# Kernel tuning notes

Measured on AMD Instinct MI355X. Metric: run time of the kernel, lower is better.

## Reference

```python
import jax, jax.numpy as jnp
import numpy as np

NUM_HEADS = 16
LN_EPS = 1e-5


def setup_inputs() -> dict:
    key = jax.random.key(0)
    ks = jax.random.split(key, 7)
    B, S, D = 4, 1024, 1024
    s_in = 1.0 / np.sqrt(D)
    return {
        "x": jax.random.normal(ks[0], (B, S, D), dtype=jnp.float32),
        # PyTorch MHA packed in-projection: [3D, D] weight, [3D] bias
        "w_qkv": jax.random.uniform(ks[1], (3 * D, D), dtype=jnp.float32, minval=-s_in, maxval=s_in),
        "b_qkv": jnp.zeros((3 * D,), dtype=jnp.float32),
        "w_out": jax.random.uniform(ks[2], (D, D), dtype=jnp.float32, minval=-s_in, maxval=s_in),
        "b_out": jnp.zeros((D,), dtype=jnp.float32),
        "ln_w": jnp.ones((D,), dtype=jnp.float32),
        "ln_b": jnp.zeros((D,), dtype=jnp.float32),
    }


def _layernorm(x, w, b):
    m = jnp.mean(x, axis=-1, keepdims=True)
    v = jnp.var(x, axis=-1, keepdims=True)
    return (x - m) * jax.lax.rsqrt(v + LN_EPS) * w + b


def reference(x, w_qkv, b_qkv, w_out, b_out, ln_w, ln_b):
    B, S, D = x.shape
    H = NUM_HEADS
    hd = D // H
    # packed QKV projection (torch: F.linear(x, w_qkv, b_qkv) then chunk)
    qkv = x @ w_qkv.T + b_qkv                      # [B, S, 3D]
    q, k, v = jnp.split(qkv, 3, axis=-1)
    q = q.reshape(B, S, H, hd).transpose(0, 2, 1, 3) * (hd ** -0.5)  # [B,H,S,hd]
    k = k.reshape(B, S, H, hd).transpose(0, 2, 1, 3)
    v = v.reshape(B, S, H, hd).transpose(0, 2, 1, 3)
    scores = jnp.einsum('bhqd,bhkd->bhqk', q, k)   # [B,H,S,S]
    attn = jax.nn.softmax(scores, axis=-1)
    ctx = jnp.einsum('bhqk,bhkd->bhqd', attn, v)   # [B,H,S,hd]
    ctx = ctx.transpose(0, 2, 1, 3).reshape(B, S, D)
    attn_out = ctx @ w_out.T + b_out
    # torch returns head-averaged weights (average_attn_weights=True)
    attn_weights = attn.mean(axis=1)               # [B,S,S]
    # dropout rate 0.0 -> identity; residual + LayerNorm
    y = _layernorm(x + attn_out, ln_w, ln_b)
    return y, attn_weights
```

## Files before the change

kernel.cpp:

```cpp
#include <hip/hip_runtime.h>
#include <cstdint>

typedef __bf16 bf16;
typedef __bf16 bf16x8 __attribute__((ext_vector_type(8)));
typedef __bf16 bf16x4 __attribute__((ext_vector_type(4)));
typedef float  f32x4  __attribute__((ext_vector_type(4)));

#define MFMA_BF16(a, b, c) __builtin_amdgcn_mfma_f32_16x16x32_bf16(a, b, c, 0, 0, 0)

#define WAITCNT_VM(n) asm volatile("s_waitcnt vmcnt(" #n ")" ::: "memory")
#define CFENCE()      asm volatile("" ::: "memory")

__device__ __forceinline__ void async_load16(const void* g, void* l) {
    __builtin_amdgcn_global_load_lds(
        (__attribute__((address_space(1))) uint32_t*)(uintptr_t)g,
        (__attribute__((address_space(3))) uint32_t*)(uint32_t)(uintptr_t)l,
        16, 0, 0);
}

__global__ void cvt3_kernel(const float* __restrict__ s0, bf16* __restrict__ d0, int n0,
                            const float* __restrict__ s1, bf16* __restrict__ d1, int n1) {
    int i = blockIdx.x * blockDim.x + threadIdx.x;
    const float* s; bf16* d; int j = i;
    if (j < n0) { s = s0; d = d0; }
    else { j -= n0; if (j >= n1) return; s = s1; d = d1; }
    float4 v = ((const float4*)s)[j];
    bf16x4 o;
    o[0] = (bf16)v.x; o[1] = (bf16)v.y; o[2] = (bf16)v.z; o[3] = (bf16)v.w;
    ((bf16x4*)d)[j] = o;
}

__global__ __launch_bounds__(256) void gemm_qkv_kernel(
    const bf16* __restrict__ A, const bf16* __restrict__ W,
    const float* __restrict__ bias,
    bf16* __restrict__ Qb, bf16* __restrict__ Kb, bf16* __restrict__ Vt)
{
    const int Kd = 1024;
    __shared__ __attribute__((aligned(16))) bf16 smem[6 * 128 * 32];
    bf16* const sA0 = smem;
    bf16* const sB0 = smem + 3 * 4096;
    int tid = threadIdx.x, lane = tid & 63, wid = tid >> 6;
    int flat = blockIdx.y * 24 + blockIdx.x;
    int orig = (flat & 7) * 96 + (flat >> 3);
    int m0 = (orig / 24) * 128, n0 = (orig % 24) * 128;
    int srow = wid * 32 + (lane >> 2);
    int pchunk = lane & 3;
    int jchunk = pchunk ^ ((lane >> 3) & 3);
    const bf16* Ag = A + (size_t)(m0 + srow) * Kd + jchunk * 8;
    const bf16* Wg = W + (size_t)(n0 + srow) * Kd + jchunk * 8;
    int soff = srow * 32 + pchunk * 8;
    int wm = (wid & 1) * 64, wn = (wid >> 1) * 64;
    int lcol = lane & 15, quad = lane >> 4;
    int ckey = (lcol >> 1) & 3;
    f32x4 acc[4][4] = {};
#define STG_Q(buf, k0_) do { \
        async_load16(Ag + (k0_), sA0 + (buf) * 4096 + soff); \
        async_load16(Ag + (k0_) + 16 * Kd, sA0 + (buf) * 4096 + soff + 512); \
        async_load16(Wg + (k0_), sB0 + (buf) * 4096 + soff); \
        async_load16(Wg + (k0_) + 16 * Kd, sB0 + (buf) * 4096 + soff + 512); \
    } while (0)
    STG_Q(0, 0);
    STG_Q(1, 32);
    STG_Q(2, 64);
    int cur = 0;
    for (int it = 0; it < 32; ++it) {
        if (it < 30)      { WAITCNT_VM(8); }
        else if (it == 30){ WAITCNT_VM(4); }
        else              { WAITCNT_VM(0); }
        __builtin_amdgcn_s_barrier();
        CFENCE();
        const bf16* cA = sA0 + cur * 4096;
        const bf16* cB = sB0 + cur * 4096;
        bf16x8 af[4], bfr[4];
#pragma unroll
        for (int i = 0; i < 4; i++)
            af[i] = *(const bf16x8*)&cA[(wm + i * 16 + lcol) * 32 + (quad ^ ckey) * 8];
#pragma unroll
        for (int i = 0; i < 4; i++)
            bfr[i] = *(const bf16x8*)&cB[(wn + i * 16 + lcol) * 32 + (quad ^ ckey) * 8];
#pragma unroll
        for (int i = 0; i < 4; i++)
#pragma unroll
            for (int j = 0; j < 4; j++)
                acc[i][j] = MFMA_BF16(af[i], bfr[j], acc[i][j]);
        CFENCE();
        __builtin_amdgcn_s_barrier();
        if (it + 3 < 32) STG_Q(cur, (it + 3) * 32);
        cur = (cur == 2) ? 0 : cur + 1;
    }
#undef STG_Q
    const int LP = 136;
    bf16* sE = smem;
    int part = n0 >> 10;
    int h0 = (n0 & 1023) >> 6;
    int b = m0 >> 10, s0 = m0 & 1023;
    if (part == 2) {
#pragma unroll
        for (int j = 0; j < 4; j++) {
            float bv = bias[n0 + wn + j * 16 + lcol];
#pragma unroll
            for (int i = 0; i < 4; i++)
#pragma unroll
                for (int r = 0; r < 4; r++)
                    sE[(wn + j * 16 + lcol) * LP + (wm + i * 16 + quad * 4 + r)] = (bf16)(acc[i][j][r] + bv);
        }
        __syncthreads();
#pragma unroll
        for (int p = 0; p < 8; p++) {
            int c = p * 256 + tid;
            int nl = c >> 4, mc = (c & 15) * 8;
            int dd = nl & 63, h = h0 + (nl >> 6);
            *(bf16x8*)&Vt[(size_t)((b * 16 + h) * 64 + dd) * 1024 + s0 + mc] = *(const bf16x8*)&sE[nl * LP + mc];
        }
    } else {
        float scv = (part == 0) ? 0.125f : 1.0f;
        bf16* dst = (part == 0) ? Qb : Kb;
#pragma unroll
        for (int j = 0; j < 4; j++) {
            float bv = bias[n0 + wn + j * 16 + lcol];
#pragma unroll
            for (int i = 0; i < 4; i++)
#pragma unroll
                for (int r = 0; r < 4; r++)
                    sE[(wm + i * 16 + quad * 4 + r) * LP + (wn + j * 16 + lcol)] = (bf16)((acc[i][j][r] + bv) * scv);
        }
        __syncthreads();
#pragma unroll
        for (int p = 0; p < 8; p++) {
            int c = p * 256 + tid;
            int half = c >> 10, idx = c & 1023;
            int m = idx >> 3, nc = (idx & 7) * 8;
            *(bf16x8*)&dst[(size_t)((b * 16 + h0 + half) * 1024 + s0 + m) * 64 + nc] =
                *(const bf16x8*)&sE[m * LP + half * 64 + nc];
        }
    }
}

__global__ __launch_bounds__(256) void gemm_out_kernel(
    const bf16* __restrict__ A, const bf16* __restrict__ W,
    const float* __restrict__ bias, float* __restrict__ out)
{
    const int Kd = 1024;
    __shared__ bf16 sA[3][64 * 32];
    __shared__ bf16 sB[3][128 * 32];
    int tid = threadIdx.x, lane = tid & 63, wid = tid >> 6;
    int m0 = blockIdx.y * 64, n0 = blockIdx.x * 128;
    int ra = tid >> 2;
    int pchunk = tid & 3;
    int jchunk = pchunk ^ ((tid >> 3) & 3);
    const bf16* Ag = A + (size_t)(m0 + ra) * Kd + jchunk * 8;
    const bf16* Wg = W + (size_t)(n0 + ra) * Kd + jchunk * 8;
    int aoff = ra * 32 + pchunk * 8;
    int wm = (wid & 1) * 32, wn = (wid >> 1) * 64;
    int lcol = lane & 15, quad = lane >> 4;
    int ckey = (lcol >> 1) & 3;
    f32x4 acc[2][4] = {};
#define STG_O(buf, k0_) do { \
        async_load16(Ag + (k0_), &sA[buf][aoff]); \
        async_load16(Wg + (k0_), &sB[buf][aoff]); \
        async_load16(Wg + (k0_) + 64 * Kd, &sB[buf][aoff + 64 * 32]); \
    } while (0)
    STG_O(0, 0);
    STG_O(1, 32);
    STG_O(2, 64);
    int cur = 0;
    for (int it = 0; it < 32; ++it) {
        if (it < 30)      { WAITCNT_VM(6); }
        else if (it == 30){ WAITCNT_VM(3); }
        else              { WAITCNT_VM(0); }
        __builtin_amdgcn_s_barrier();
        CFENCE();
        const bf16* cA = sA[cur];
        const bf16* cB = sB[cur];
        bf16x8 af[2], bfr[4];
#pragma unroll
        for (int i = 0; i < 2; i++)
            af[i] = *(const bf16x8*)&cA[(wm + i * 16 + lcol) * 32 + (quad ^ ckey) * 8];
#pragma unroll
        for (int j = 0; j < 4; j++)
            bfr[j] = *(const bf16x8*)&cB[(wn + j * 16 + lcol) * 32 + (quad ^ ckey) * 8];
#pragma unroll
        for (int i = 0; i < 2; i++)
#pragma unroll
            for (int j = 0; j < 4; j++)
                acc[i][j] = MFMA_BF16(af[i], bfr[j], acc[i][j]);
        CFENCE();
        __builtin_amdgcn_s_barrier();
        if (it + 3 < 32) STG_O(cur, (it + 3) * 32);
        cur = (cur == 2) ? 0 : cur + 1;
    }
#undef STG_O
#pragma unroll
    for (int j = 0; j < 4; j++) {
        int n = n0 + wn + j * 16 + lcol;
        float bv = bias[n];
#pragma unroll
        for (int i = 0; i < 2; i++) {
            int m = m0 + wm + i * 16 + quad * 4;
#pragma unroll
            for (int r = 0; r < 4; r++) out[(size_t)(m + r) * 1024 + n] = acc[i][j][r] + bv;
        }
    }
}

__global__ __launch_bounds__(512) void flash_kernel(
    const bf16* __restrict__ Qb, const bf16* __restrict__ Kb, const bf16* __restrict__ Vt,
    bf16* __restrict__ ctx, float* __restrict__ ml)
{
    __shared__ bf16 sK[2][64 * 64];
    __shared__ bf16 sV[2][64 * 64];
    __shared__ bf16 pt[8][16 * 64];
    int tid = threadIdx.x, lane = tid & 63, wid = tid >> 6;
    int bx = blockIdx.x;
    int orig = (bx & 7) * 64 + (bx >> 3);
    int qt = orig & 7;
    int h = (orig >> 3) & 15;
    int b = orig >> 7;
    int lcol = lane & 15, quad = lane >> 4;
    size_t base = (size_t)(b * 16 + h) * 65536;

    int q0 = qt * 128 + wid * 16;
    const bf16* qp = Qb + base + (size_t)(q0 + lcol) * 64 + quad * 8;
    bf16x8 a0 = *(const bf16x8*)qp;
    bf16x8 a1 = *(const bf16x8*)(qp + 32);

    char* wpt = (char*)&pt[wid][0];
    int sr = tid >> 3;
    int pp = tid & 7;
    int jj = pp ^ (sr & 7);
    int sw = lcol & 7;

#define STAGE_KV(buf, kt_) do { \
        async_load16(Kb + base + (size_t)((kt_) * 64 + sr) * 64 + jj * 8, &sK[buf][sr * 64 + pp * 8]); \
        async_load16(Vt + base + (size_t)sr * 1024 + (kt_) * 64 + jj * 8, &sV[buf][sr * 64 + pp * 8]); \
    } while (0)

    float l_[4] = {0.f, 0.f, 0.f, 0.f};
    f32x4 o[4] = {};

    STAGE_KV(0, 0);
    int cur = 0;
    for (int kt = 0; kt < 16; kt++) {
        __syncthreads();
        if (kt < 15) STAGE_KV(cur ^ 1, kt + 1);
        const bf16* sKc = &sK[cur][0];
        const bf16* sVc = &sV[cur][0];
#pragma unroll
        for (int nt = 0; nt < 4; nt++) {
            int ck = quad ^ sw;
            bf16x8 bk0 = *(const bf16x8*)&sKc[(nt * 16 + lcol) * 64 + ck * 8];
            bf16x8 bk1 = *(const bf16x8*)&sKc[(nt * 16 + lcol) * 64 + (ck ^ 4) * 8];
            f32x4 s = {};
            s = MFMA_BF16(a0, bk0, s);
            s = MFMA_BF16(a1, bk1, s);
#pragma unroll
            for (int rr = 0; rr < 4; rr++) {
                float p = __expf(s[rr]);
                l_[rr] += p;
                int row = quad * 4 + rr;
                *(bf16*)(wpt + row * 128 + ((nt * 32 + lcol * 2) ^ ((row & 7) << 4))) = (bf16)p;
            }
        }
#pragma unroll
        for (int kf = 0; kf < 2; kf++) {
            bf16x8 pa = *(const bf16x8*)(wpt + lcol * 128 + (((kf * 4 + quad) ^ sw) << 4));
#pragma unroll
            for (int dt = 0; dt < 4; dt++) {
                bf16x8 vb = *(const bf16x8*)&sVc[(dt * 16 + lcol) * 64 + ((kf * 4 + quad) ^ sw) * 8];
                o[dt] = MFMA_BF16(pa, vb, o[dt]);
            }
        }
        cur ^= 1;
    }
#undef STAGE_KV
#pragma unroll
    for (int mk = 1; mk < 16; mk <<= 1)
#pragma unroll
        for (int rr = 0; rr < 4; rr++) l_[rr] += __shfl_xor(l_[rr], mk, 64);
#pragma unroll
    for (int rr = 0; rr < 4; rr++) {
        float inv = 1.f / l_[rr];
        int row = quad * 4 + rr;
#pragma unroll
        for (int dt = 0; dt < 4; dt++)
            *(bf16*)(wpt + row * 128 + ((dt * 32 + lcol * 2) ^ ((row & 7) << 4))) = (bf16)(o[dt][rr] * inv);
        if (lcol == 0)
            ml[(size_t)(b * 16 + h) * 1024 + q0 + row] = l_[rr];
    }
    int r8a = lane >> 3, ca = lane & 7;
#pragma unroll
    for (int half = 0; half < 2; half++) {
        int r8 = r8a + half * 8;
        bf16x8 v = *(const bf16x8*)(wpt + r8 * 128 + ((ca * 16) ^ ((r8 & 7) << 4)));
        *(bf16x8*)&ctx[(size_t)(b * 1024 + q0 + r8) * 1024 + h * 64 + ca * 8] = v;
    }
}

__global__ __launch_bounds__(512) void aw_kernel(
    const bf16* __restrict__ Qb, const bf16* __restrict__ Kb,
    const float* __restrict__ ml, float* __restrict__ aw,
    const float* __restrict__ wof, bf16* __restrict__ wob)
{
    __shared__ bf16 sK[2][64 * 64];
    int tid = threadIdx.x, lane = tid & 63, wid = tid >> 6;
    int bx = blockIdx.x;
    if (bx >= 512) {
        int i = (bx - 512) * 512 + tid;
        float4 v = ((const float4*)wof)[i];
        bf16x4 o;
        o[0] = (bf16)v.x; o[1] = (bf16)v.y; o[2] = (bf16)v.z; o[3] = (bf16)v.w;
        ((bf16x4*)wob)[i] = o;
        return;
    }
    int orig = (bx & 7) * 64 + (bx >> 3);
    int kt = orig & 15;
    int qt = (orig >> 4) & 7;
    int b = orig >> 7;
    int lcol = lane & 15, quad = lane >> 4;
    int q0 = qt * 128 + wid * 16;
    int kbase = kt * 64;
    int sw = lcol & 7;
    int sr = tid >> 3, pp = tid & 7, jj = pp ^ (sr & 7);

#define STAGE_K(buf, hh) \
        async_load16(Kb + (size_t)(b * 16 + (hh)) * 65536 + (size_t)(kbase + sr) * 64 + jj * 8, \
                     &sK[buf][sr * 64 + pp * 8])

    float acc[16];
#pragma unroll
    for (int i = 0; i < 16; i++) acc[i] = 0.f;

    bf16x8 a0c, a1c, a0n, a1n;
    float4 mvC, mvN;
    {
        const bf16* qp = Qb + (size_t)(b * 16) * 65536 + (size_t)(q0 + lcol) * 64 + quad * 8;
        a0c = *(const bf16x8*)qp;
        a1c = *(const bf16x8*)(qp + 32);
        mvC = *(const float4*)(ml + (size_t)(b * 16) * 1024 + q0 + quad * 4);
    }
    STAGE_K(0, 0);
    int cur = 0;
    for (int h = 0; h < 16; h++) {
        __syncthreads();
        if (h < 15) {
            STAGE_K(cur ^ 1, h + 1);
            const bf16* qp = Qb + (size_t)(b * 16 + h + 1) * 65536 + (size_t)(q0 + lcol) * 64 + quad * 8;
            a0n = *(const bf16x8*)qp;
            a1n = *(const bf16x8*)(qp + 32);
            mvN = *(const float4*)(ml + (size_t)(b * 16 + h + 1) * 1024 + q0 + quad * 4);
        }
        float scale[4] = {0.0625f / mvC.x, 0.0625f / mvC.y, 0.0625f / mvC.z, 0.0625f / mvC.w};
#pragma unroll
        for (int nt = 0; nt < 4; nt++) {
            int ck = quad ^ sw;
            bf16x8 bk0 = *(const bf16x8*)&sK[cur][(nt * 16 + lcol) * 64 + ck * 8];
            bf16x8 bk1 = *(const bf16x8*)&sK[cur][(nt * 16 + lcol) * 64 + (ck ^ 4) * 8];
            f32x4 s = {};
            s = MFMA_BF16(a0c, bk0, s);
            s = MFMA_BF16(a1c, bk1, s);
#pragma unroll
            for (int rr = 0; rr < 4; rr++)
                acc[nt * 4 + rr] += __expf(s[rr]) * scale[rr];
        }
        if (h < 15) { a0c = a0n; a1c = a1n; mvC = mvN; }
        cur ^= 1;
    }
#undef STAGE_K
#pragma unroll
    for (int nt = 0; nt < 4; nt++)
#pragma unroll
        for (int rr = 0; rr < 4; rr++)
            aw[(size_t)(b * 1024 + q0 + quad * 4 + rr) * 1024 + kbase + nt * 16 + lcol] = acc[nt * 4 + rr];
}

__global__ __launch_bounds__(256) void ln_kernel(
    const float* __restrict__ x, const float* __restrict__ ao,
    const float* __restrict__ w, const float* __restrict__ bsh,
    float* __restrict__ y)
{
    int row = blockIdx.x, tid = threadIdx.x;
    float4 xv = ((const float4*)(x + (size_t)row * 1024))[tid];
    float4 av = ((const float4*)(ao + (size_t)row * 1024))[tid];
    float4 v = {xv.x + av.x, xv.y + av.y, xv.z + av.z, xv.w + av.w};
    float s = v.x + v.y + v.z + v.w;
    float ss = v.x * v.x + v.y * v.y + v.z * v.z + v.w * v.w;
#pragma unroll
    for (int off = 32; off; off >>= 1) { s += __shfl_down(s, off); ss += __shfl_down(ss, off); }
    __shared__ float rs[4], rss[4];
    int lane = tid & 63, wid = tid >> 6;
    if (lane == 0) { rs[wid] = s; rss[wid] = ss; }
    __syncthreads();
    s = rs[0] + rs[1] + rs[2] + rs[3];
    ss = rss[0] + rss[1] + rss[2] + rss[3];
    float mean = s * (1.f / 1024.f);
    float var = ss * (1.f / 1024.f) - mean * mean;
    float inv = rsqrtf(var + 1e-5f);
    float4 wv = ((const float4*)w)[tid];
    float4 bv = ((const float4*)bsh)[tid];
    float4 o;
    o.x = (v.x - mean) * inv * wv.x + bv.x;
    o.y = (v.y - mean) * inv * wv.y + bv.y;
    o.z = (v.z - mean) * inv * wv.z + bv.z;
    o.w = (v.w - mean) * inv * wv.w + bv.w;
    ((float4*)y)[row * 256 + tid] = o;
}

extern "C" void kernel_launch(void* const* d_in, const int* in_sizes, int n_in,
                              void* d_out, int out_size, void* d_ws, size_t ws_size,
                              hipStream_t stream) {
    const float* x     = (const float*)d_in[0];
    const float* w_qkv = (const float*)d_in[1];
    const float* b_qkv = (const float*)d_in[2];
    const float* w_out = (const float*)d_in[3];
    const float* b_out = (const float*)d_in[4];
    const float* ln_w  = (const float*)d_in[5];
    const float* ln_b  = (const float*)d_in[6];

    char* ws = (char*)d_ws;
    bf16*   Qb    = (bf16*)(ws);
    bf16*   Kb    = (bf16*)(ws + (8ull  << 20));
    bf16*   Vt    = (bf16*)(ws + (16ull << 20));
    bf16*   ctx   = (bf16*)(ws + (24ull << 20));
    float*  ml    = (float*)(ws + (32ull << 20));
    bf16*   x_bf  = (bf16*)(ws + (33ull << 20));
    bf16*   wq_bf = (bf16*)(ws + (41ull << 20));
    bf16*   wo_bf = (bf16*)(ws + (16ull << 20));
    float*  ao    = (float*)(ws);

    float* y_out  = (float*)d_out;
    float* aw_out = y_out + 4ull * 1024 * 1024;

    cvt3_kernel<<<7168, 256, 0, stream>>>(x, x_bf, 1048576, w_qkv, wq_bf, 786432);
    gemm_qkv_kernel<<<dim3(24, 32), 256, 0, stream>>>(x_bf, wq_bf, b_qkv, Qb, Kb, Vt);
    flash_kernel<<<512, 512, 0, stream>>>(Qb, Kb, Vt, ctx, ml);
    aw_kernel<<<1024, 512, 0, stream>>>(Qb, Kb, ml, aw_out, w_out, wo_bf);
    gemm_out_kernel<<<dim3(8, 64), 256, 0, stream>>>(ctx, wo_bf, b_out, ao);
    ln_kernel<<<4096, 256, 0, stream>>>(x, ao, ln_w, ln_b, y_out);
}
```

Before: 201.2 us.

## Fuse output projection GEMM into attention-weights kernel and move w_out conversion

```diff
diff --git a/kernel.cpp b/kernel.cpp
--- a/kernel.cpp
+++ b/kernel.cpp
@@ -136,172 +136,14 @@
     }
 }
 
-__global__ __launch_bounds__(256) void gemm_out_kernel(
-    const bf16* __restrict__ A, const bf16* __restrict__ W,
-    const float* __restrict__ bias, float* __restrict__ out)
-{
-    const int Kd = 1024;
-    __shared__ bf16 sA[3][64 * 32];
-    __shared__ bf16 sB[3][128 * 32];
-    int tid = threadIdx.x, lane = tid & 63, wid = tid >> 6;
-    int m0 = blockIdx.y * 64, n0 = blockIdx.x * 128;
-    int ra = tid >> 2;
-    int pchunk = tid & 3;
-    int jchunk = pchunk ^ ((tid >> 3) & 3);
-    const bf16* Ag = A + (size_t)(m0 + ra) * Kd + jchunk * 8;
-    const bf16* Wg = W + (size_t)(n0 + ra) * Kd + jchunk * 8;
-    int aoff = ra * 32 + pchunk * 8;
-    int wm = (wid & 1) * 32, wn = (wid >> 1) * 64;
-    int lcol = lane & 15, quad = lane >> 4;
-    int ckey = (lcol >> 1) & 3;
-    f32x4 acc[2][4] = {};
-#define STG_O(buf, k0_) do { \
-        async_load16(Ag + (k0_), &sA[buf][aoff]); \
-        async_load16(Wg + (k0_), &sB[buf][aoff]); \
-        async_load16(Wg + (k0_) + 64 * Kd, &sB[buf][aoff + 64 * 32]); \
-    } while (0)
-    STG_O(0, 0);
-    STG_O(1, 32);
-    STG_O(2, 64);
-    int cur = 0;
-    for (int it = 0; it < 32; ++it) {
-        if (it < 30)      { WAITCNT_VM(6); }
-        else if (it == 30){ WAITCNT_VM(3); }
-        else              { WAITCNT_VM(0); }
-        __builtin_amdgcn_s_barrier();
-        CFENCE();
-        const bf16* cA = sA[cur];
-        const bf16* cB = sB[cur];
-        bf16x8 af[2], bfr[4];
-#pragma unroll
-        for (int i = 0; i < 2; i++)
-            af[i] = *(const bf16x8*)&cA[(wm + i * 16 + lcol) * 32 + (quad ^ ckey) * 8];
-#pragma unroll
-        for (int j = 0; j < 4; j++)
-            bfr[j] = *(const bf16x8*)&cB[(wn + j * 16 + lcol) * 32 + (quad ^ ckey) * 8];
-#pragma unroll
-        for (int i = 0; i < 2; i++)
-#pragma unroll
-            for (int j = 0; j < 4; j++)
-                acc[i][j] = MFMA_BF16(af[i], bfr[j], acc[i][j]);
-        CFENCE();
-        __builtin_amdgcn_s_barrier();
-        if (it + 3 < 32) STG_O(cur, (it + 3) * 32);
-        cur = (cur == 2) ? 0 : cur + 1;
-    }
-#undef STG_O
-#pragma unroll
-    for (int j = 0; j < 4; j++) {
-        int n = n0 + wn + j * 16 + lcol;
-        float bv = bias[n];
-#pragma unroll
-        for (int i = 0; i < 2; i++) {
-            int m = m0 + wm + i * 16 + quad * 4;
-#pragma unroll
-            for (int r = 0; r < 4; r++) out[(size_t)(m + r) * 1024 + n] = acc[i][j][r] + bv;
-        }
-    }
-}
-
 __global__ __launch_bounds__(512) void flash_kernel(
     const bf16* __restrict__ Qb, const bf16* __restrict__ Kb, const bf16* __restrict__ Vt,
-    bf16* __restrict__ ctx, float* __restrict__ ml)
+    bf16* __restrict__ ctx, float* __restrict__ ml,
+    const float* __restrict__ wof, bf16* __restrict__ wob)
 {
     __shared__ bf16 sK[2][64 * 64];
     __shared__ bf16 sV[2][64 * 64];
     __shared__ bf16 pt[8][16 * 64];
-    int tid = threadIdx.x, lane = tid & 63, wid = tid >> 6;
-    int bx = blockIdx.x;
-    int orig = (bx & 7) * 64 + (bx >> 3);
-    int qt = orig & 7;
-    int h = (orig >> 3) & 15;
-    int b = orig >> 7;
-    int lcol = lane & 15, quad = lane >> 4;
-    size_t base = (size_t)(b * 16 + h) * 65536;
-
-    int q0 = qt * 128 + wid * 16;
-    const bf16* qp = Qb + base + (size_t)(q0 + lcol) * 64 + quad * 8;
-    bf16x8 a0 = *(const bf16x8*)qp;
-    bf16x8 a1 = *(const bf16x8*)(qp + 32);
-
-    char* wpt = (char*)&pt[wid][0];
-    int sr = tid >> 3;
-    int pp = tid & 7;
-    int jj = pp ^ (sr & 7);
-    int sw = lcol & 7;
-
-#define STAGE_KV(buf, kt_) do { \
-        async_load16(Kb + base + (size_t)((kt_) * 64 + sr) * 64 + jj * 8, &sK[buf][sr * 64 + pp * 8]); \
-        async_load16(Vt + base + (size_t)sr * 1024 + (kt_) * 64 + jj * 8, &sV[buf][sr * 64 + pp * 8]); \
-    } while (0)
-
-    float l_[4] = {0.f, 0.f, 0.f, 0.f};
-    f32x4 o[4] = {};
-
-    STAGE_KV(0, 0);
-    int cur = 0;
-    for (int kt = 0; kt < 16; kt++) {
-        __syncthreads();
-        if (kt < 15) STAGE_KV(cur ^ 1, kt + 1);
-        const bf16* sKc = &sK[cur][0];
-        const bf16* sVc = &sV[cur][0];
-#pragma unroll
-        for (int nt = 0; nt < 4; nt++) {
-            int ck = quad ^ sw;
-            bf16x8 bk0 = *(const bf16x8*)&sKc[(nt * 16 + lcol) * 64 + ck * 8];
-            bf16x8 bk1 = *(const bf16x8*)&sKc[(nt * 16 + lcol) * 64 + (ck ^ 4) * 8];
-            f32x4 s = {};
-            s = MFMA_BF16(a0, bk0, s);
-            s = MFMA_BF16(a1, bk1, s);
-#pragma unroll
-            for (int rr = 0; rr < 4; rr++) {
-                float p = __expf(s[rr]);
-                l_[rr] += p;
-                int row = quad * 4 + rr;
-                *(bf16*)(wpt + row * 128 + ((nt * 32 + lcol * 2) ^ ((row & 7) << 4))) = (bf16)p;
-            }
-        }
-#pragma unroll
-        for (int kf = 0; kf < 2; kf++) {
-            bf16x8 pa = *(const bf16x8*)(wpt + lcol * 128 + (((kf * 4 + quad) ^ sw) << 4));
-#pragma unroll
-            for (int dt = 0; dt < 4; dt++) {
-                bf16x8 vb = *(const bf16x8*)&sVc[(dt * 16 + lcol) * 64 + ((kf * 4 + quad) ^ sw) * 8];
-                o[dt] = MFMA_BF16(pa, vb, o[dt]);
-            }
-        }
-        cur ^= 1;
-    }
-#undef STAGE_KV
-#pragma unroll
-    for (int mk = 1; mk < 16; mk <<= 1)
-#pragma unroll
-        for (int rr = 0; rr < 4; rr++) l_[rr] += __shfl_xor(l_[rr], mk, 64);
-#pragma unroll
-    for (int rr = 0; rr < 4; rr++) {
-        float inv = 1.f / l_[rr];
-        int row = quad * 4 + rr;
-#pragma unroll
-        for (int dt = 0; dt < 4; dt++)
-            *(bf16*)(wpt + row * 128 + ((dt * 32 + lcol * 2) ^ ((row & 7) << 4))) = (bf16)(o[dt][rr] * inv);
-        if (lcol == 0)
-            ml[(size_t)(b * 16 + h) * 1024 + q0 + row] = l_[rr];
-    }
-    int r8a = lane >> 3, ca = lane & 7;
-#pragma unroll
-    for (int half = 0; half < 2; half++) {
-        int r8 = r8a + half * 8;
-        bf16x8 v = *(const bf16x8*)(wpt + r8 * 128 + ((ca * 16) ^ ((r8 & 7) << 4)));
-        *(bf16x8*)&ctx[(size_t)(b * 1024 + q0 + r8) * 1024 + h * 64 + ca * 8] = v;
-    }
-}
-
-__global__ __launch_bounds__(512) void aw_kernel(
-    const bf16* __restrict__ Qb, const bf16* __restrict__ Kb,
-    const float* __restrict__ ml, float* __restrict__ aw,
-    const float* __restrict__ wof, bf16* __restrict__ wob)
-{
-    __shared__ bf16 sK[2][64 * 64];
     int tid = threadIdx.x, lane = tid & 63, wid = tid >> 6;
     int bx = blockIdx.x;
     if (bx >= 512) {
@@ -313,10 +155,168 @@
         return;
     }
     int orig = (bx & 7) * 64 + (bx >> 3);
+    int qt = orig & 7;
+    int h = (orig >> 3) & 15;
+    int b = orig >> 7;
+    int lcol = lane & 15, quad = lane >> 4;
+    size_t base = (size_t)(b * 16 + h) * 65536;
+
+    int q0 = qt * 128 + wid * 16;
+    const bf16* qp = Qb + base + (size_t)(q0 + lcol) * 64 + quad * 8;
+    bf16x8 a0 = *(const bf16x8*)qp;
+    bf16x8 a1 = *(const bf16x8*)(qp + 32);
+
+    char* wpt = (char*)&pt[wid][0];
+    int sr = tid >> 3;
+    int pp = tid & 7;
+    int jj = pp ^ (sr & 7);
+    int sw = lcol & 7;
+
+#define STAGE_KV(buf, kt_) do { \
+        async_load16(Kb + base + (size_t)((kt_) * 64 + sr) * 64 + jj * 8, &sK[buf][sr * 64 + pp * 8]); \
+        async_load16(Vt + base + (size_t)sr * 1024 + (kt_) * 64 + jj * 8, &sV[buf][sr * 64 + pp * 8]); \
+    } while (0)
+
+    float l_[4] = {0.f, 0.f, 0.f, 0.f};
+    f32x4 o[4] = {};
+
+    STAGE_KV(0, 0);
+    int cur = 0;
+    for (int kt = 0; kt < 16; kt++) {
+        __syncthreads();
+        if (kt < 15) STAGE_KV(cur ^ 1, kt + 1);
+        const bf16* sKc = &sK[cur][0];
+        const bf16* sVc = &sV[cur][0];
+#pragma unroll
+        for (int nt = 0; nt < 4; nt++) {
+            int ck = quad ^ sw;
+            bf16x8 bk0 = *(const bf16x8*)&sKc[(nt * 16 + lcol) * 64 + ck * 8];
+            bf16x8 bk1 = *(const bf16x8*)&sKc[(nt * 16 + lcol) * 64 + (ck ^ 4) * 8];
+            f32x4 s = {};
+            s = MFMA_BF16(a0, bk0, s);
+            s = MFMA_BF16(a1, bk1, s);
+#pragma unroll
+            for (int rr = 0; rr < 4; rr++) {
+                float p = __expf(s[rr]);
+                l_[rr] += p;
+                int row = quad * 4 + rr;
+                *(bf16*)(wpt + row * 128 + ((nt * 32 + lcol * 2) ^ ((row & 7) << 4))) = (bf16)p;
+            }
+        }
+#pragma unroll
+        for (int kf = 0; kf < 2; kf++) {
+            bf16x8 pa = *(const bf16x8*)(wpt + lcol * 128 + (((kf * 4 + quad) ^ sw) << 4));
+#pragma unroll
+            for (int dt = 0; dt < 4; dt++) {
+                bf16x8 vb = *(const bf16x8*)&sVc[(dt * 16 + lcol) * 64 + ((kf * 4 + quad) ^ sw) * 8];
+                o[dt] = MFMA_BF16(pa, vb, o[dt]);
+            }
+        }
+        cur ^= 1;
+    }
+#undef STAGE_KV
+#pragma unroll
+    for (int mk = 1; mk < 16; mk <<= 1)
+#pragma unroll
+        for (int rr = 0; rr < 4; rr++) l_[rr] += __shfl_xor(l_[rr], mk, 64);
+#pragma unroll
+    for (int rr = 0; rr < 4; rr++) {
+        float inv = 1.f / l_[rr];
+        int row = quad * 4 + rr;
+#pragma unroll
+        for (int dt = 0; dt < 4; dt++)
+            *(bf16*)(wpt + row * 128 + ((dt * 32 + lcol * 2) ^ ((row & 7) << 4))) = (bf16)(o[dt][rr] * inv);
+        if (lcol == 0)
+            ml[(size_t)(b * 16 + h) * 1024 + q0 + row] = l_[rr];
+    }
+    int r8a = lane >> 3, ca = lane & 7;
+#pragma unroll
+    for (int half = 0; half < 2; half++) {
+        int r8 = r8a + half * 8;
+        bf16x8 v = *(const bf16x8*)(wpt + r8 * 128 + ((ca * 16) ^ ((r8 & 7) << 4)));
+        *(bf16x8*)&ctx[(size_t)(b * 1024 + q0 + r8) * 1024 + h * 64 + ca * 8] = v;
+    }
+}
+
+__global__ __launch_bounds__(512) void awo_kernel(
+    const bf16* __restrict__ Qb, const bf16* __restrict__ Kb,
+    const float* __restrict__ ml, float* __restrict__ aw,
+    const bf16* __restrict__ ctx, const bf16* __restrict__ wob,
+    const float* __restrict__ bias, float* __restrict__ yao)
+{
+    __shared__ __attribute__((aligned(16))) bf16 smem[6 * 128 * 32];
+    int tid = threadIdx.x, lane = tid & 63, wid = tid >> 6;
+    int bx = blockIdx.x;
+    int lcol = lane & 15, quad = lane >> 4;
+
+    if (bx >= 512) {
+        const int Kd = 1024;
+        bf16* const sA0 = smem;
+        bf16* const sB0 = smem + 3 * 4096;
+        int obx = bx - 512;
+        int m0 = (obx >> 3) * 128, n0 = (obx & 7) * 128;
+        int srow = tid >> 2;
+        int pchunk = tid & 3;
+        int jchunk = pchunk ^ ((tid >> 3) & 3);
+        const bf16* Ag = ctx + (size_t)(m0 + srow) * Kd + jchunk * 8;
+        const bf16* Wg = wob + (size_t)(n0 + srow) * Kd + jchunk * 8;
+        int soff = srow * 32 + pchunk * 8;
+        int wm = (wid & 3) * 32, wn = (wid >> 2) * 64;
+        int ckey = (lcol >> 1) & 3;
+        f32x4 acc[2][4] = {};
+#define STG_O(buf, k0_) do { \
+        async_load16(Ag + (k0_), sA0 + (buf) * 4096 + soff); \
+        async_load16(Wg + (k0_), sB0 + (buf) * 4096 + soff); \
+    } while (0)
+        STG_O(0, 0);
+        STG_O(1, 32);
+        STG_O(2, 64);
+        int cur = 0;
+        for (int it = 0; it < 32; ++it) {
+            if (it < 30)      { WAITCNT_VM(4); }
+            else if (it == 30){ WAITCNT_VM(2); }
+            else              { WAITCNT_VM(0); }
+            __builtin_amdgcn_s_barrier();
+            CFENCE();
+            const bf16* cA = sA0 + cur * 4096;
+            const bf16* cB = sB0 + cur * 4096;
+            bf16x8 af[2], bfr[4];
+#pragma unroll
+            for (int i = 0; i < 2; i++)
+                af[i] = *(const bf16x8*)&cA[(wm + i * 16 + lcol) * 32 + (quad ^ ckey) * 8];
+#pragma unroll
+            for (int j = 0; j < 4; j++)
+                bfr[j] = *(const bf16x8*)&cB[(wn + j * 16 + lcol) * 32 + (quad ^ ckey) * 8];
+#pragma unroll
+            for (int i = 0; i < 2; i++)
+#pragma unroll
+                for (int j = 0; j < 4; j++)
+                    acc[i][j] = MFMA_BF16(af[i], bfr[j], acc[i][j]);
+            CFENCE();
+            __builtin_amdgcn_s_barrier();
+            if (it + 3 < 32) STG_O(cur, (it + 3) * 32);
+            cur = (cur == 2) ? 0 : cur + 1;
+        }
+#undef STG_O
+#pragma unroll
+        for (int j = 0; j < 4; j++) {
+            int n = n0 + wn + j * 16 + lcol;
+            float bv = bias[n];
+#pragma unroll
+            for (int i = 0; i < 2; i++) {
+                int m = m0 + wm + i * 16 + quad * 4;
+#pragma unroll
+                for (int r = 0; r < 4; r++) yao[(size_t)(m + r) * 1024 + n] = acc[i][j][r] + bv;
+            }
+        }
+        return;
+    }
+
+    bf16* const sK0 = smem;
+    int orig = (bx & 7) * 64 + (bx >> 3);
     int kt = orig & 15;
     int qt = (orig >> 4) & 7;
     int b = orig >> 7;
-    int lcol = lane & 15, quad = lane >> 4;
     int q0 = qt * 128 + wid * 16;
     int kbase = kt * 64;
     int sw = lcol & 7;
@@ -324,7 +324,7 @@
 
 #define STAGE_K(buf, hh) \
         async_load16(Kb + (size_t)(b * 16 + (hh)) * 65536 + (size_t)(kbase + sr) * 64 + jj * 8, \
-                     &sK[buf][sr * 64 + pp * 8])
+                     sK0 + (buf) * 4096 + sr * 64 + pp * 8)
 
     float acc[16];
 #pragma unroll
@@ -350,11 +350,12 @@
             mvN = *(const float4*)(ml + (size_t)(b * 16 + h + 1) * 1024 + q0 + quad * 4);
         }
         float scale[4] = {0.0625f / mvC.x, 0.0625f / mvC.y, 0.0625f / mvC.z, 0.0625f / mvC.w};
+        const bf16* sKc = sK0 + cur * 4096;
 #pragma unroll
         for (int nt = 0; nt < 4; nt++) {
             int ck = quad ^ sw;
-            bf16x8 bk0 = *(const bf16x8*)&sK[cur][(nt * 16 + lcol) * 64 + ck * 8];
-            bf16x8 bk1 = *(const bf16x8*)&sK[cur][(nt * 16 + lcol) * 64 + (ck ^ 4) * 8];
+            bf16x8 bk0 = *(const bf16x8*)&sKc[(nt * 16 + lcol) * 64 + ck * 8];
+            bf16x8 bk1 = *(const bf16x8*)&sKc[(nt * 16 + lcol) * 64 + (ck ^ 4) * 8];
             f32x4 s = {};
             s = MFMA_BF16(a0c, bk0, s);
             s = MFMA_BF16(a1c, bk1, s);
@@ -424,16 +425,15 @@
     float*  ml    = (float*)(ws + (32ull << 20));
     bf16*   x_bf  = (bf16*)(ws + (33ull << 20));
     bf16*   wq_bf = (bf16*)(ws + (41ull << 20));
-    bf16*   wo_bf = (bf16*)(ws + (16ull << 20));
-    float*  ao    = (float*)(ws);
+    bf16*   wo_bf = (bf16*)(ws + (33ull << 20));
 
     float* y_out  = (float*)d_out;
     float* aw_out = y_out + 4ull * 1024 * 1024;
+    float* ao     = y_out;
 
     cvt3_kernel<<<7168, 256, 0, stream>>>(x, x_bf, 1048576, w_qkv, wq_bf, 786432);
     gemm_qkv_kernel<<<dim3(24, 32), 256, 0, stream>>>(x_bf, wq_bf, b_qkv, Qb, Kb, Vt);
-    flash_kernel<<<512, 512, 0, stream>>>(Qb, Kb, Vt, ctx, ml);
-    aw_kernel<<<1024, 512, 0, stream>>>(Qb, Kb, ml, aw_out, w_out, wo_bf);
-    gemm_out_kernel<<<dim3(8, 64), 256, 0, stream>>>(ctx, wo_bf, b_out, ao);
+    flash_kernel<<<1024, 512, 0, stream>>>(Qb, Kb, Vt, ctx, ml, w_out, wo_bf);
+    awo_kernel<<<768, 512, 0, stream>>>(Qb, Kb, ml, aw_out, ctx, wo_bf, b_out, ao);
     ln_kernel<<<4096, 256, 0, stream>>>(x, ao, ln_w, ln_b, y_out);
 }
```

Measured after the change: 192.8 us. -4.2%, faster.
